# Kernel tuning notes

Measured on AMD Instinct MI355X. Metric: run time of the kernel, lower is better.

The kernel has to match this reference:

```python
import jax, jax.numpy as jnp
import numpy as np

EPS_S = 1e-06
EPS_R = 1e-06

def _gaussian_masks(mu, logsx, logsy, rho, H, W, dtype):
    # coordinate grid in [-1,1], grid[h,w] = (x, y)
    ys = jnp.linspace(-1.0, 1.0, H, dtype=dtype)
    xs = jnp.linspace(-1.0, 1.0, W, dtype=dtype)
    Y, X = jnp.meshgrid(ys, xs, indexing='ij')  # [H,W]
    sx = jnp.exp(logsx)[:, None, None] + EPS_S   # [n,1,1]
    sy = jnp.exp(logsy)[:, None, None] + EPS_S
    r = jnp.tanh(rho)[:, None, None]
    xc = (X[None] - mu[:, 0, None, None]) / sx   # [n,H,W]
    yc = (Y[None] - mu[:, 1, None, None]) / sy
    A = xc ** 2 + yc ** 2 - 2.0 * r * xc * yc
    denom = 2.0 * (1.0 - r ** 2 + EPS_R)
    return jnp.exp(-A / denom)                   # [n,H,W]

def setup_inputs() -> dict:
    key = jax.random.key(0)
    ks = jax.random.split(key, 6)
    B, C, H, W, n = 32, 256, 36, 64, 4096
    feat = jax.random.normal(ks[0], (B, C, H, W), dtype=jnp.float32)
    mu = jax.random.uniform(ks[1], (n, 2), dtype=jnp.float32) * 2.0 - 1.0
    logsx = jnp.zeros((n,), dtype=jnp.float32)
    logsy = jnp.zeros((n,), dtype=jnp.float32)
    rho = jnp.zeros((n,), dtype=jnp.float32)
    weight = jax.random.normal(ks[5], (n, C), dtype=jnp.float32) * 0.01
    return {"feat": feat, "mu": mu, "logsx": logsx, "logsy": logsy, "rho": rho, "weight": weight}

def reference(feat, mu, logsx, logsy, rho, weight):
    B, C, H, W = feat.shape
    G = _gaussian_masks(mu, logsx, logsy, rho, H, W, feat.dtype)  # [n,H,W]
    # pooled[b,n,c] = sum_{h,w} feat[b,c,h,w] * G[n,h,w]  (batched GEMM)
    pooled = jnp.einsum('bchw,nhw->bnc', feat, G)
    out = jnp.einsum('bnc,nc->bn', pooled, weight.astype(feat.dtype))
    return out
```

## Files before the change

### kernel.cpp

```cpp
#include <hip/hip_runtime.h>
#include <hip/hip_bf16.h>

#define P_HW   2304
#define NG     4096
#define NCOL   8192
#define KDIM   P_HW

typedef __bf16 bf16x8 __attribute__((ext_vector_type(8)));
typedef float  f32x4  __attribute__((ext_vector_type(4)));

__device__ __forceinline__ unsigned short f2bf(float f) {
    union { float f; unsigned int u; } x; x.f = f;
    unsigned int r = x.u + 0x7FFFu + ((x.u >> 16) & 1u);
    return (unsigned short)(r >> 16);
}

__global__ void mask_kernel(const float* __restrict__ mu,
                            const float* __restrict__ logsx,
                            const float* __restrict__ logsy,
                            const float* __restrict__ rho,
                            unsigned short* __restrict__ G) {
    const int n = blockIdx.x;
    const float mux = mu[2 * n], muy = mu[2 * n + 1];
    const float sx = __expf(logsx[n]) + 1e-6f;
    const float sy = __expf(logsy[n]) + 1e-6f;
    const float r  = tanhf(rho[n]);
    const float inv_den = 1.0f / (2.0f * (1.0f - r * r + 1e-6f));
    const float isx = 1.0f / sx, isy = 1.0f / sy;
    for (int p = threadIdx.x; p < P_HW; p += 256) {
        const int h = p >> 6, w = p & 63;
        const float X = -1.0f + (float)w * (2.0f / 63.0f);
        const float Y = -1.0f + (float)h * (2.0f / 35.0f);
        const float xc = (X - mux) * isx;
        const float yc = (Y - muy) * isy;
        const float A = xc * xc + yc * yc - 2.0f * r * xc * yc;
        G[(size_t)n * P_HW + p] = f2bf(__expf(-A * inv_den));
    }
}

__global__ void cast_feat(const float* __restrict__ feat,
                          unsigned short* __restrict__ F) {
    const size_t i = ((size_t)blockIdx.x * 256 + threadIdx.x) * 8;
    const float4 v0 = *(const float4*)(feat + i);
    const float4 v1 = *(const float4*)(feat + i + 4);
    union { unsigned short s[8]; uint4 q; } o;
    o.s[0] = f2bf(v0.x); o.s[1] = f2bf(v0.y); o.s[2] = f2bf(v0.z); o.s[3] = f2bf(v0.w);
    o.s[4] = f2bf(v1.x); o.s[5] = f2bf(v1.y); o.s[6] = f2bf(v1.z); o.s[7] = f2bf(v1.w);
    *(uint4*)(F + i) = o.q;
}

__device__ __forceinline__ void async16(const void* g, void* l) {
    __builtin_amdgcn_global_load_lds(
        (__attribute__((address_space(1))) void*)(unsigned long long)g,
        (__attribute__((address_space(3))) void*)(unsigned int)(unsigned long long)l,
        16, 0, 0);
}

__global__ __launch_bounds__(256) void gemm_fused(
    const unsigned short* __restrict__ G,
    const unsigned short* __restrict__ F,
    const float* __restrict__ weight,
    float* __restrict__ out)
{
    __shared__ __align__(16) unsigned short ldsA[128 * 32];
    __shared__ __align__(16) unsigned short ldsB[128 * 32];

    const int tid  = threadIdx.x;
    const int lane = tid & 63;
    const int wave = tid >> 6;
    const int waveM = wave >> 1, waveN = wave & 1;
    const int quad = lane >> 4, m = lane & 15;

    const int rowBase = blockIdx.y * 128;
    const int colBase = blockIdx.x * 128;

    const int idx0 = tid, idx1 = tid + 256;
    const int r0 = idx0 >> 2, c0 = (idx0 & 3) * 8;
    const int r1 = idx1 >> 2, c1 = (idx1 & 3) * 8;

    const unsigned short* Ag0 = G + (size_t)(rowBase + r0) * KDIM + c0;
    const unsigned short* Ag1 = G + (size_t)(rowBase + r1) * KDIM + c1;
    const unsigned short* Bg0 = F + (size_t)(colBase + r0) * KDIM + c0;
    const unsigned short* Bg1 = F + (size_t)(colBase + r1) * KDIM + c1;

    f32x4 acc[4][4];
#pragma unroll
    for (int i = 0; i < 4; ++i)
#pragma unroll
        for (int j = 0; j < 4; ++j)
            acc[i][j] = (f32x4){0.f, 0.f, 0.f, 0.f};

    for (int k0 = 0; k0 < KDIM; k0 += 32) {
        async16(Ag0 + k0, &ldsA[idx0 * 8]);
        async16(Ag1 + k0, &ldsA[idx1 * 8]);
        async16(Bg0 + k0, &ldsB[idx0 * 8]);
        async16(Bg1 + k0, &ldsB[idx1 * 8]);
        __syncthreads();

        bf16x8 a[4], b[4];
#pragma unroll
        for (int i = 0; i < 4; ++i)
            a[i] = *(const bf16x8*)&ldsA[(waveM * 64 + i * 16 + m) * 32 + quad * 8];
#pragma unroll
        for (int j = 0; j < 4; ++j)
            b[j] = *(const bf16x8*)&ldsB[(waveN * 64 + j * 16 + m) * 32 + quad * 8];

#pragma unroll
        for (int i = 0; i < 4; ++i)
#pragma unroll
            for (int j = 0; j < 4; ++j)
                acc[i][j] = __builtin_amdgcn_mfma_f32_16x16x32_bf16(a[i], b[j], acc[i][j], 0, 0, 0);
        __syncthreads();
    }

    const int bidx  = colBase >> 8;
    const int cwave = (colBase & 255) + waveN * 64;
#pragma unroll
    for (int i = 0; i < 4; ++i) {
        const int nrow = rowBase + waveM * 64 + i * 16 + quad * 4;
#pragma unroll
        for (int reg = 0; reg < 4; ++reg) {
            const float* wrow = weight + (size_t)(nrow + reg) * 256 + cwave + m;
            float s = acc[i][0][reg] * wrow[0]
                    + acc[i][1][reg] * wrow[16]
                    + acc[i][2][reg] * wrow[32]
                    + acc[i][3][reg] * wrow[48];
            s += __shfl_xor(s, 1);
            s += __shfl_xor(s, 2);
            s += __shfl_xor(s, 4);
            s += __shfl_xor(s, 8);
            if (m == 0)
                atomicAdd(out + (size_t)bidx * NG + nrow + reg, s);
        }
    }
}

extern "C" void kernel_launch(void* const* d_in, const int* in_sizes, int n_in,
                              void* d_out, int out_size, void* d_ws, size_t ws_size,
                              hipStream_t stream) {
    const float* feat   = (const float*)d_in[0];
    const float* mu     = (const float*)d_in[1];
    const float* logsx  = (const float*)d_in[2];
    const float* logsy  = (const float*)d_in[3];
    const float* rho    = (const float*)d_in[4];
    const float* weight = (const float*)d_in[5];
    float* out = (float*)d_out;

    unsigned short* Gbuf = (unsigned short*)d_ws;
    unsigned short* Fbuf = Gbuf + (size_t)NG * P_HW;

    hipMemsetAsync(out, 0, (size_t)32 * NG * sizeof(float), stream);

    hipLaunchKernelGGL(mask_kernel, dim3(NG), dim3(256), 0, stream,
                       mu, logsx, logsy, rho, Gbuf);

    hipLaunchKernelGGL(cast_feat, dim3(9216), dim3(256), 0, stream, feat, Fbuf);

    hipLaunchKernelGGL(gemm_fused, dim3(NCOL / 128, NG / 128), dim3(256), 0, stream,
                       Gbuf, Fbuf, weight, out);
}
```

Measured before the change: 316.7 us.

## Double GEMM K-tile to 64 with XOR-swizzled LDS and vectorize mask stores

The GEMM main loop now stages 64-wide K tiles instead of 32, halving the number of barrier pairs per tile, and issues four async loads per matrix per thread. The LDS layout applies an XOR swizzle on 16-byte chunks by row to avoid bank conflicts on the MFMA fragment reads. The mask kernel now computes eight consecutive pixels per thread and writes them as one 16-byte store. LDS use doubles, which could lower occupancy, and there is still no double buffering.

Measured after the change: 312.8 us. Within noise of the previous version (-1.2%).

```diff
diff --git a/kernel.cpp b/kernel.cpp
--- a/kernel.cpp
+++ b/kernel.cpp
@@ -27,14 +27,19 @@
     const float r  = tanhf(rho[n]);
     const float inv_den = 1.0f / (2.0f * (1.0f - r * r + 1e-6f));
     const float isx = 1.0f / sx, isy = 1.0f / sy;
-    for (int p = threadIdx.x; p < P_HW; p += 256) {
-        const int h = p >> 6, w = p & 63;
-        const float X = -1.0f + (float)w * (2.0f / 63.0f);
-        const float Y = -1.0f + (float)h * (2.0f / 35.0f);
-        const float xc = (X - mux) * isx;
+    for (int base = threadIdx.x * 8; base < P_HW; base += 2048) {
+        const int h = base >> 6, w0 = base & 63;
+        const float Y  = -1.0f + (float)h * (2.0f / 35.0f);
         const float yc = (Y - muy) * isy;
-        const float A = xc * xc + yc * yc - 2.0f * r * xc * yc;
-        G[(size_t)n * P_HW + p] = f2bf(__expf(-A * inv_den));
+        union { unsigned short s[8]; uint4 q; } o;
+#pragma unroll
+        for (int j = 0; j < 8; ++j) {
+            const float X  = -1.0f + (float)(w0 + j) * (2.0f / 63.0f);
+            const float xc = (X - mux) * isx;
+            const float A  = xc * xc + yc * yc - 2.0f * r * xc * yc;
+            o.s[j] = f2bf(__expf(-A * inv_den));
+        }
+        *(uint4*)&G[(size_t)n * P_HW + base] = o.q;
     }
 }
 
@@ -62,8 +67,8 @@
     const float* __restrict__ weight,
     float* __restrict__ out)
 {
-    __shared__ __align__(16) unsigned short ldsA[128 * 32];
-    __shared__ __align__(16) unsigned short ldsB[128 * 32];
+    __shared__ __align__(16) unsigned short ldsA[128 * 64];
+    __shared__ __align__(16) unsigned short ldsB[128 * 64];
 
     const int tid  = threadIdx.x;
     const int lane = tid & 63;
@@ -74,14 +79,19 @@
     const int rowBase = blockIdx.y * 128;
     const int colBase = blockIdx.x * 128;
 
-    const int idx0 = tid, idx1 = tid + 256;
-    const int r0 = idx0 >> 2, c0 = (idx0 & 3) * 8;
-    const int r1 = idx1 >> 2, c1 = (idx1 & 3) * 8;
-
-    const unsigned short* Ag0 = G + (size_t)(rowBase + r0) * KDIM + c0;
-    const unsigned short* Ag1 = G + (size_t)(rowBase + r1) * KDIM + c1;
-    const unsigned short* Bg0 = F + (size_t)(colBase + r0) * KDIM + c0;
-    const unsigned short* Bg1 = F + (size_t)(colBase + r1) * KDIM + c1;
+    const unsigned short* Aptr[4];
+    const unsigned short* Bptr[4];
+    int ldsOff[4];
+#pragma unroll
+    for (int i = 0; i < 4; ++i) {
+        const int s  = i * 256 + tid;
+        const int r  = s >> 3;
+        const int cp = s & 7;
+        const int c  = cp ^ (r & 7);
+        Aptr[i] = G + (size_t)(rowBase + r) * KDIM + c * 8;
+        Bptr[i] = F + (size_t)(colBase + r) * KDIM + c * 8;
+        ldsOff[i] = s * 8;
+    }
 
     f32x4 acc[4][4];
 #pragma unroll
@@ -90,26 +100,34 @@
         for (int j = 0; j < 4; ++j)
             acc[i][j] = (f32x4){0.f, 0.f, 0.f, 0.f};
 
-    for (int k0 = 0; k0 < KDIM; k0 += 32) {
-        async16(Ag0 + k0, &ldsA[idx0 * 8]);
-        async16(Ag1 + k0, &ldsA[idx1 * 8]);
-        async16(Bg0 + k0, &ldsB[idx0 * 8]);
-        async16(Bg1 + k0, &ldsB[idx1 * 8]);
+    for (int k0 = 0; k0 < KDIM; k0 += 64) {
+#pragma unroll
+        for (int i = 0; i < 4; ++i) async16(Aptr[i] + k0, &ldsA[ldsOff[i]]);
+#pragma unroll
+        for (int i = 0; i < 4; ++i) async16(Bptr[i] + k0, &ldsB[ldsOff[i]]);
         __syncthreads();
 
-        bf16x8 a[4], b[4];
 #pragma unroll
-        for (int i = 0; i < 4; ++i)
-            a[i] = *(const bf16x8*)&ldsA[(waveM * 64 + i * 16 + m) * 32 + quad * 8];
+        for (int h = 0; h < 2; ++h) {
+            bf16x8 a[4], b[4];
 #pragma unroll
-        for (int j = 0; j < 4; ++j)
-            b[j] = *(const bf16x8*)&ldsB[(waveN * 64 + j * 16 + m) * 32 + quad * 8];
-
+            for (int i = 0; i < 4; ++i) {
+                const int r  = waveM * 64 + i * 16 + m;
+                const int cp = (h * 4 + quad) ^ (r & 7);
+                a[i] = *(const bf16x8*)&ldsA[r * 64 + cp * 8];
+            }
 #pragma unroll
-        for (int i = 0; i < 4; ++i)
+            for (int j = 0; j < 4; ++j) {
+                const int r  = waveN * 64 + j * 16 + m;
+                const int cp = (h * 4 + quad) ^ (r & 7);
+                b[j] = *(const bf16x8*)&ldsB[r * 64 + cp * 8];
+            }
 #pragma unroll
-            for (int j = 0; j < 4; ++j)
-                acc[i][j] = __builtin_amdgcn_mfma_f32_16x16x32_bf16(a[i], b[j], acc[i][j], 0, 0, 0);
+            for (int i = 0; i < 4; ++i)
+#pragma unroll
+                for (int j = 0; j < 4; ++j)
+                    acc[i][j] = __builtin_amdgcn_mfma_f32_16x16x32_bf16(a[i], b[j], acc[i][j], 0, 0, 0);
+        }
         __syncthreads();
     }
 
```
